# Optimization experiments

Measured on AMD Instinct MI355X. Metric: run time of the kernel, lower is better.

## Reference

```python
import jax, jax.numpy as jnp
import numpy as np

N_KERNELS = 16
KSIZE = 3
B, H, W = 16, 512, 512

def setup_inputs() -> dict:
    key = jax.random.key(0)
    k1, k2, k3, k4 = jax.random.split(key, 4)
    x = jax.random.uniform(k1, (B, 1, H, W), dtype=jnp.float32)
    kernels = jax.random.normal(k2, (N_KERNELS, 1, KSIZE, KSIZE), dtype=jnp.float32)
    reactants = jax.random.normal(k3, (N_KERNELS,), dtype=jnp.float32)
    products = jax.random.normal(k4, (N_KERNELS,), dtype=jnp.float32)
    return {"x": x, "kernels": kernels, "reactants": reactants, "products": products}

def reference(x, kernels, reactants, products):
    # All n_kernels 1->1 convs batched as a single 1->n_kernels conv.
    pad = KSIZE // 2
    N = jax.lax.conv_general_dilated(
        x, kernels,
        window_strides=(1, 1),
        padding=[(pad, pad), (pad, pad)],
        dimension_numbers=("NCHW", "OIHW", "NCHW"),
    )  # [B, n_kernels, H, W]
    GAIN = 10.0
    condition = jax.nn.sigmoid(GAIN * (N - reactants[None, :, None, None]))
    # x has 1 channel; broadcasts against the n_kernels axis
    update = condition * (products[None, :, None, None] - x)
    delta = jnp.sum(update, axis=1, keepdims=True)  # sum over kernels -> [B,1,H,W]
    return jnp.clip(x + delta, 0.0, 1.0)
```

## Files before the change

kernel.cpp:

```cpp
#include <hip/hip_runtime.h>


#define NK 16
#define BATCH 16
#define H 512
#define W 512
#define GAIN 10.0f

__global__ __launch_bounds__(256) void nca_kernel(
    const float* __restrict__ x,
    const float* __restrict__ kernels,
    const float* __restrict__ reactants,
    const float* __restrict__ products,
    float* __restrict__ out)
{
    const int idx = blockIdx.x * blockDim.x + threadIdx.x;
    const int w4 = (idx & 127) << 2;
    const int h  = (idx >> 7) & 511;
    const int b  = idx >> 16;

    const float* xb = x + (size_t)b * H * W;

    float v[3][6];
#pragma unroll
    for (int r = 0; r < 3; ++r) {
        const int row = h + r - 1;
        if (row >= 0 && row < H) {
            const float* xr = xb + row * W;
            const float4 c = *(const float4*)(xr + w4);
            v[r][1] = c.x; v[r][2] = c.y; v[r][3] = c.z; v[r][4] = c.w;
            v[r][0] = (w4 > 0)     ? xr[w4 - 1] : 0.0f;
            v[r][5] = (w4 + 4 < W) ? xr[w4 + 4] : 0.0f;
        } else {
#pragma unroll
            for (int c = 0; c < 6; ++c) v[r][c] = 0.0f;
        }
    }

    float s0[4] = {0.f, 0.f, 0.f, 0.f};
    float s1[4] = {0.f, 0.f, 0.f, 0.f};

    for (int k = 0; k < NK; ++k) {
        float wk[9];
#pragma unroll
        for (int i = 0; i < 9; ++i) wk[i] = kernels[k * 9 + i];
        const float c0 = -GAIN * reactants[k];
        const float pk = products[k];

#pragma unroll
        for (int p = 0; p < 4; ++p) {
            float n = 0.0f;
#pragma unroll
            for (int r = 0; r < 3; ++r)
#pragma unroll
                for (int c = 0; c < 3; ++c)
                    n = fmaf(v[r][p + c], wk[r * 3 + c], n);
            const float z = fmaf(GAIN, n, c0);
            const float e = __expf(-z);
            const float sig = __builtin_amdgcn_rcpf(1.0f + e);
            s0[p] += sig;
            s1[p] = fmaf(sig, pk, s1[p]);
        }
    }

    float4 o;
    float* op = &o.x;
#pragma unroll
    for (int p = 0; p < 4; ++p) {
        const float xv = v[1][p + 1];
        float res = xv + s1[p] - xv * s0[p];
        res = fminf(fmaxf(res, 0.0f), 1.0f);
        op[p] = res;
    }
    *(float4*)(out + (size_t)idx * 4) = o;
}

extern "C" void kernel_launch(void* const* d_in, const int* in_sizes, int n_in,
                              void* d_out, int out_size, void* d_ws, size_t ws_size,
                              hipStream_t stream) {
    const float* x         = (const float*)d_in[0];
    const float* kernels   = (const float*)d_in[1];
    const float* reactants = (const float*)d_in[2];
    const float* products  = (const float*)d_in[3];
    float* out = (float*)d_out;

    const int total_strips = BATCH * H * (W / 4);
    nca_kernel<<<total_strips / 256, 256, 0, stream>>>(x, kernels, reactants, products, out);
}
```

Baseline: 101.9 us.

## Compute 2x4 output tile per thread, fold gain into exp2, use constant address space

```diff
diff --git a/kernel.cpp b/kernel.cpp
--- a/kernel.cpp
+++ b/kernel.cpp
@@ -5,7 +5,15 @@
 #define BATCH 16
 #define H 512
 #define W 512
-#define GAIN 10.0f
+#define G2 14.4269504088896340f
+
+#if __has_builtin(__builtin_amdgcn_exp2f)
+#define EXP2F(x) __builtin_amdgcn_exp2f(x)
+#else
+#define EXP2F(x) exp2f(x)
+#endif
+
+typedef const __attribute__((address_space(4))) float cfloat;
 
 __global__ __launch_bounds__(256) void nca_kernel(
     const float* __restrict__ x,
@@ -16,15 +24,15 @@
 {
     const int idx = blockIdx.x * blockDim.x + threadIdx.x;
     const int w4 = (idx & 127) << 2;
-    const int h  = (idx >> 7) & 511;
-    const int b  = idx >> 16;
+    const int h0 = ((idx >> 7) & 255) << 1;
+    const int b  = idx >> 15;
 
-    const float* xb = x + (size_t)b * H * W;
+    const float* xb = x + (size_t)b * (H * W);
 
-    float v[3][6];
+    float v[4][6];
 #pragma unroll
-    for (int r = 0; r < 3; ++r) {
-        const int row = h + r - 1;
+    for (int r = 0; r < 4; ++r) {
+        const int row = h0 + r - 1;
         if (row >= 0 && row < H) {
             const float* xr = xb + row * W;
             const float4 c = *(const float4*)(xr + w4);
@@ -37,42 +45,52 @@
         }
     }
 
-    float s0[4] = {0.f, 0.f, 0.f, 0.f};
-    float s1[4] = {0.f, 0.f, 0.f, 0.f};
+    cfloat* kc = (cfloat*)kernels;
+    cfloat* rc = (cfloat*)reactants;
+    cfloat* pc = (cfloat*)products;
 
+    float s0[2][4] = {{0.f,0.f,0.f,0.f},{0.f,0.f,0.f,0.f}};
+    float s1[2][4] = {{0.f,0.f,0.f,0.f},{0.f,0.f,0.f,0.f}};
+
+#pragma unroll
     for (int k = 0; k < NK; ++k) {
         float wk[9];
 #pragma unroll
-        for (int i = 0; i < 9; ++i) wk[i] = kernels[k * 9 + i];
-        const float c0 = -GAIN * reactants[k];
-        const float pk = products[k];
+        for (int i = 0; i < 9; ++i) wk[i] = kc[k * 9 + i];
+        const float c2 = G2 * rc[k];
+        const float pk = pc[k];
 
 #pragma unroll
-        for (int p = 0; p < 4; ++p) {
-            float n = 0.0f;
+        for (int py = 0; py < 2; ++py) {
 #pragma unroll
-            for (int r = 0; r < 3; ++r)
+            for (int p = 0; p < 4; ++p) {
+                float n = 0.0f;
 #pragma unroll
-                for (int c = 0; c < 3; ++c)
-                    n = fmaf(v[r][p + c], wk[r * 3 + c], n);
-            const float z = fmaf(GAIN, n, c0);
-            const float e = __expf(-z);
-            const float sig = __builtin_amdgcn_rcpf(1.0f + e);
-            s0[p] += sig;
-            s1[p] = fmaf(sig, pk, s1[p]);
+                for (int r = 0; r < 3; ++r)
+#pragma unroll
+                    for (int c = 0; c < 3; ++c)
+                        n = fmaf(v[py + r][p + c], wk[r * 3 + c], n);
+                const float t = fmaf(-G2, n, c2);
+                const float e = EXP2F(t);
+                const float sig = __builtin_amdgcn_rcpf(1.0f + e);
+                s0[py][p] += sig;
+                s1[py][p] = fmaf(sig, pk, s1[py][p]);
+            }
         }
     }
 
-    float4 o;
-    float* op = &o.x;
 #pragma unroll
-    for (int p = 0; p < 4; ++p) {
-        const float xv = v[1][p + 1];
-        float res = xv + s1[p] - xv * s0[p];
-        res = fminf(fmaxf(res, 0.0f), 1.0f);
-        op[p] = res;
+    for (int py = 0; py < 2; ++py) {
+        float4 o;
+        float* op = &o.x;
+#pragma unroll
+        for (int p = 0; p < 4; ++p) {
+            const float xv = v[py + 1][p + 1];
+            float res = xv + s1[py][p] - xv * s0[py][p];
+            op[p] = fminf(fmaxf(res, 0.0f), 1.0f);
+        }
+        *(float4*)(out + ((size_t)(b * H + h0 + py) * W + w4)) = o;
     }
-    *(float4*)(out + (size_t)idx * 4) = o;
 }
 
 extern "C" void kernel_launch(void* const* d_in, const int* in_sizes, int n_in,
@@ -84,6 +102,6 @@
     const float* products  = (const float*)d_in[3];
     float* out = (float*)d_out;
 
-    const int total_strips = BATCH * H * (W / 4);
-    nca_kernel<<<total_strips / 256, 256, 0, stream>>>(x, kernels, reactants, products, out);
+    const int total_tiles = BATCH * (H / 2) * (W / 4);
+    nca_kernel<<<total_tiles / 256, 256, 0, stream>>>(x, kernels, reactants, products, out);
 }
```

Result: no change. 100.2 us (-1.6%).
